# Performance work log

Measured on AMD Instinct MI355X. Metric: run time of the kernel, lower is better.

## Reference

```python
import jax, jax.numpy as jnp
import numpy as np

K = 7          # involution kernel size
G = 16         # groups = channels // group_channels = 256 // 16
BN_EPS = 1e-3  # Keras BatchNormalization default epsilon


def setup_inputs() -> dict:
    key = jax.random.key(0)
    ks = jax.random.split(key, 6)
    B, H, W, C = 4, 56, 56, 256
    Cr = C // 4                      # reduction_ratio = 4
    x = jax.random.normal(ks[0], (B, H, W, C), dtype=jnp.float32)
    w_reduce = jax.random.normal(ks[1], (C, Cr), dtype=jnp.float32) * (1.0 / np.sqrt(C))
    gamma = jnp.ones((Cr,), dtype=jnp.float32)
    beta = jnp.zeros((Cr,), dtype=jnp.float32)
    mean = jax.random.normal(ks[2], (Cr,), dtype=jnp.float32) * 0.1
    var = jax.random.uniform(ks[3], (Cr,), dtype=jnp.float32) + 0.5
    w_span = jax.random.normal(ks[4], (Cr, K * K * G), dtype=jnp.float32) * (1.0 / np.sqrt(Cr))
    b_span = jnp.zeros((K * K * G,), dtype=jnp.float32)
    return {"x": x, "w_reduce": w_reduce, "gamma": gamma, "beta": beta,
            "mean": mean, "var": var, "w_span": w_span, "b_span": b_span}


def reference(x, w_reduce, gamma, beta, mean, var, w_span, b_span):
    B, H, W, C = x.shape
    Cg = C // G  # channels per group
    # kernel generation branch: 1x1 conv -> BN (inference) -> ReLU -> 1x1 conv
    r = jnp.einsum('bhwc,cd->bhwd', x, w_reduce)
    r = jax.nn.relu((r - mean) * (gamma / jnp.sqrt(var + BN_EPS)) + beta)
    kgen = jnp.einsum('bhwd,de->bhwe', r, w_span) + b_span      # (B,H,W,K*K*G)
    kgen = kgen.reshape(B, H, W, G, K * K)
    # im2col with SAME padding (stride=1, pad (K-1)//2 symmetric), depth order (kh, kw, C)
    p = (K - 1) // 2
    xp = jnp.pad(x, ((0, 0), (p, p), (p, p), (0, 0)))
    patches = jnp.stack([xp[:, i:i + H, j:j + W, :]
                         for i in range(K) for j in range(K)], axis=3)  # (B,H,W,K*K,C)
    patches = patches.reshape(B, H, W, K * K, G, Cg)
    # per-pixel, per-group weighted reduction over the K*K window
    out = jnp.einsum('bhwgk,bhwkgc->bhwgc', kgen, patches)
    return out.reshape(B, H, W, C)
```

## Files before the change

### kernel.cpp

```cpp
#include <hip/hip_runtime.h>
#include <hip/hip_bf16.h>
#include <stdint.h>

#define B_   4
#define H_   56
#define W_   56
#define C_   256
#define CR   64
#define G_   16
#define CG   16
#define KS   7
#define KK   49
#define PADR 3
#define NPX  (B_*H_*W_)

typedef __attribute__((ext_vector_type(8))) short bf16x8;
typedef __attribute__((ext_vector_type(4))) float f32x4;
typedef __attribute__((ext_vector_type(2))) float f32x2;

__device__ __forceinline__ uint32_t f2bf(float f) {
    uint32_t x = __float_as_uint(f);
    return (x + 0x7fffu + ((x >> 16) & 1u)) >> 16;
}
__device__ __forceinline__ uint32_t pkbf(float a, float b) {
    union { __hip_bfloat162 h; uint32_t u; } c;
    c.h = __float22bfloat162_rn(make_float2(a, b));
    return c.u;
}
__device__ __forceinline__ float blo(uint32_t w) { return __uint_as_float(w << 16); }
__device__ __forceinline__ float bhi(uint32_t w) { return __uint_as_float(w & 0xffff0000u); }

union U4V { uint4 u; bf16x8 v; };

__global__ __launch_bounds__(256) void k0_prepack(
        const float* __restrict__ wr, const float* __restrict__ wspan,
        const float* __restrict__ gamma, const float* __restrict__ beta,
        const float* __restrict__ mean, const float* __restrict__ var,
        uint16_t* __restrict__ wrp, uint16_t* __restrict__ wpp,
        float* __restrict__ scale, float* __restrict__ shift) {
    int idx = blockIdx.x * 256 + threadIdx.x;
    {
        int j = idx & 7, lane = (idx >> 3) & 63, nb = (idx >> 9) & 3,
            kb = (idx >> 11) & 1, g = idx >> 12;
        int k = kb * 32 + (lane >> 4) * 8 + j;
        int n = nb * 16 + (lane & 15);
        float v = (n < KK) ? wspan[k * (KK * G_) + g * KK + n] : 0.f;
        wpp[idx] = (uint16_t)f2bf(v);
    }
    if (idx < 16384) {
        int j = idx & 7, lane = (idx >> 3) & 63, nb = (idx >> 9) & 3, kb = idx >> 11;
        int k = kb * 32 + (lane >> 4) * 8 + j;
        int n = nb * 16 + (lane & 15);
        wrp[idx] = (uint16_t)f2bf(wr[k * CR + n]);
    }
    if (idx < CR) {
        float s = gamma[idx] * rsqrtf(var[idx] + 1e-3f);
        scale[idx] = s;
        shift[idx] = beta[idx] - mean[idx] * s;
    }
}

__global__ __launch_bounds__(64) void k1_reduce(
        const float* __restrict__ x, const uint16_t* __restrict__ wrp,
        const float* __restrict__ scale, const float* __restrict__ shift,
        uint16_t* __restrict__ r) {
    int lane = threadIdx.x;
    int mt = blockIdx.x;
    int pix = mt * 16 + (lane & 15);
    const float* xrow = x + (size_t)pix * C_ + (lane >> 4) * 8;
    f32x4 acc[4] = {{0,0,0,0},{0,0,0,0},{0,0,0,0},{0,0,0,0}};
    for (int kb = 0; kb < 8; ++kb) {
        float4 a0 = *(const float4*)(xrow + kb * 32);
        float4 a1 = *(const float4*)(xrow + kb * 32 + 4);
        U4V af;
        af.u = make_uint4(pkbf(a0.x, a0.y), pkbf(a0.z, a0.w),
                          pkbf(a1.x, a1.y), pkbf(a1.z, a1.w));
        const uint16_t* wb = wrp + kb * 2048 + lane * 8;
        #pragma unroll
        for (int nb = 0; nb < 4; ++nb) {
            bf16x8 bf_ = *(const bf16x8*)(wb + nb * 512);
            acc[nb] = __builtin_amdgcn_mfma_f32_16x16x32_bf16(af.v, bf_, acc[nb], 0, 0, 0);
        }
    }
    int rq = (lane >> 4) * 4;
    #pragma unroll
    for (int nb = 0; nb < 4; ++nb) {
        int d = nb * 16 + (lane & 15);
        float s = scale[d], sh = shift[d];
        #pragma unroll
        for (int rg = 0; rg < 4; ++rg) {
            float v = fmaf(acc[nb][rg], s, sh);
            v = v > 0.f ? v : 0.f;
            r[(size_t)(mt * 16 + rq + rg) * CR + d] = (uint16_t)f2bf(v);
        }
    }
}

#define TS   14
#define HS   20
#define XSW  24
#define XROW (21*XSW)
#define KGW  56

__global__ __launch_bounds__(256, 3) void k2_involution(
        const float* __restrict__ x, const uint16_t* __restrict__ r,
        const uint16_t* __restrict__ wpp, const float* __restrict__ bspan,
        float* __restrict__ out) {
    __shared__ __align__(16) uint16_t xs[HS * XROW];
    __shared__ __align__(16) uint16_t kg[208 * KGW];

    int tid  = threadIdx.x;
    int tile = blockIdx.x, g = blockIdx.y, b = blockIdx.z;
    int ty0 = (tile >> 2) * TS, tx0 = (tile & 3) * TS;

    #pragma unroll
    for (int pass = 0; pass < 2; ++pass) {
        int i = tid + pass * 256;
        if (i < HS * HS) {
            int py = i / HS, px = i % HS;
            int gy = ty0 + py - PADR, gx = tx0 + px - PADR;
            uint4 wA = make_uint4(0, 0, 0, 0), wB = wA;
            if (gy >= 0 && gy < H_ && gx >= 0 && gx < W_) {
                const float* xp = x + (((size_t)(b * H_ + gy)) * W_ + gx) * C_ + g * CG;
                float4 v0 = *(const float4*)(xp + 0);
                float4 v1 = *(const float4*)(xp + 4);
                float4 v2 = *(const float4*)(xp + 8);
                float4 v3 = *(const float4*)(xp + 12);
                wA = make_uint4(pkbf(v0.x, v0.y), pkbf(v0.z, v0.w),
                                pkbf(v1.x, v1.y), pkbf(v1.z, v1.w));
                wB = make_uint4(pkbf(v2.x, v2.y), pkbf(v2.z, v2.w),
                                pkbf(v3.x, v3.y), pkbf(v3.z, v3.w));
            }
            uint16_t* dst = xs + py * XROW + px * XSW;
            *(uint4*)(dst + 0) = wA;
            *(uint4*)(dst + 8) = wB;
        }
    }

    int lane = tid & 63, w = tid >> 6;
    bf16x8 bfr[2][4];
    const uint16_t* wb = wpp + g * 4096 + lane * 8;
    #pragma unroll
    for (int kb = 0; kb < 2; ++kb)
        #pragma unroll
        for (int nb = 0; nb < 4; ++nb)
            bfr[kb][nb] = *(const bf16x8*)(wb + kb * 2048 + nb * 512);
    float bias[4];
    #pragma unroll
    for (int nb = 0; nb < 4; ++nb) {
        int n = nb * 16 + (lane & 15);
        bias[nb] = (n < KK) ? bspan[g * KK + n] : 0.f;
    }
    for (int mi = 0; mi < 4; ++mi) {
        int mt = mi * 4 + w;
        if (mt < 13) {
            int m  = mt * 16 + (lane & 15);
            int mm = m < 196 ? m : 195;
            int ly = mm / TS, lx = mm % TS;
            size_t pix = ((size_t)(b * H_ + ty0 + ly)) * W_ + (tx0 + lx);
            const uint16_t* rp = r + pix * CR + (lane >> 4) * 8;
            bf16x8 a0 = *(const bf16x8*)(rp);
            bf16x8 a1 = *(const bf16x8*)(rp + 32);
            f32x4 acc[4];
            #pragma unroll
            for (int nb = 0; nb < 4; ++nb)
                acc[nb] = (f32x4){bias[nb], bias[nb], bias[nb], bias[nb]};
            #pragma unroll
            for (int nb = 0; nb < 4; ++nb) {
                acc[nb] = __builtin_amdgcn_mfma_f32_16x16x32_bf16(a0, bfr[0][nb], acc[nb], 0, 0, 0);
                acc[nb] = __builtin_amdgcn_mfma_f32_16x16x32_bf16(a1, bfr[1][nb], acc[nb], 0, 0, 0);
            }
            #pragma unroll
            for (int nb = 0; nb < 4; ++nb) {
                int n = nb * 16 + (lane & 15);
                if (n < KK) {
                    int row = mt * 16 + (lane >> 4) * 4;
                    #pragma unroll
                    for (int rg = 0; rg < 4; ++rg)
                        kg[(row + rg) * KGW + n] = (uint16_t)f2bf(acc[nb][rg]);
                }
            }
        }
    }
    __syncthreads();

    if (tid < 196) {
        int p = tid >> 1, h = tid & 1;
        int ty = p / 7, tx = (p % 7) * 2;
        int rowL = ty * TS + tx;

        uint32_t kwL[28], kwR[28];
        #pragma unroll
        for (int t = 0; t < 7; ++t) {
            uint4 a = *(const uint4*)(kg + rowL * KGW + t * 8);
            uint4 c = *(const uint4*)(kg + (rowL + 1) * KGW + t * 8);
            kwL[t*4+0] = a.x; kwL[t*4+1] = a.y; kwL[t*4+2] = a.z; kwL[t*4+3] = a.w;
            kwR[t*4+0] = c.x; kwR[t*4+1] = c.y; kwR[t*4+2] = c.z; kwR[t*4+3] = c.w;
        }

        f32x2 accL[4] = {{0,0},{0,0},{0,0},{0,0}};
        f32x2 accR[4] = {{0,0},{0,0},{0,0},{0,0}};
        #pragma unroll
        for (int kh = 0; kh < KS; ++kh) {
            const uint16_t* xrow = xs + (ty + kh) * XROW + tx * XSW + h * 8;
            #pragma unroll
            for (int j = 0; j < 8; ++j) {
                uint4 xw = *(const uint4*)(xrow + j * XSW);
                float kvL = 0.f, kvR = 0.f;
                if (j < 7) { int t = kh * 7 + j;     kvL = (t & 1) ? bhi(kwL[t>>1]) : blo(kwL[t>>1]); }
                if (j > 0) { int t = kh * 7 + j - 1; kvR = (t & 1) ? bhi(kwR[t>>1]) : blo(kwR[t>>1]); }
                f32x2 kL = {kvL, kvL}, kR = {kvR, kvR};
                f32x2 x0 = {blo(xw.x), bhi(xw.x)};
                f32x2 x1 = {blo(xw.y), bhi(xw.y)};
                f32x2 x2 = {blo(xw.z), bhi(xw.z)};
                f32x2 x3 = {blo(xw.w), bhi(xw.w)};
                accL[0] = __builtin_elementwise_fma(kL, x0, accL[0]);
                accL[1] = __builtin_elementwise_fma(kL, x1, accL[1]);
                accL[2] = __builtin_elementwise_fma(kL, x2, accL[2]);
                accL[3] = __builtin_elementwise_fma(kL, x3, accL[3]);
                accR[0] = __builtin_elementwise_fma(kR, x0, accR[0]);
                accR[1] = __builtin_elementwise_fma(kR, x1, accR[1]);
                accR[2] = __builtin_elementwise_fma(kR, x2, accR[2]);
                accR[3] = __builtin_elementwise_fma(kR, x3, accR[3]);
            }
        }
        size_t pixL = ((size_t)(b * H_ + ty0 + ty)) * W_ + (tx0 + tx);
        float* opL = out + pixL * C_ + g * CG + h * 8;
        float* opR = opL + C_;
        *(float4*)(opL + 0) = make_float4(accL[0].x, accL[0].y, accL[1].x, accL[1].y);
        *(float4*)(opL + 4) = make_float4(accL[2].x, accL[2].y, accL[3].x, accL[3].y);
        *(float4*)(opR + 0) = make_float4(accR[0].x, accR[0].y, accR[1].x, accR[1].y);
        *(float4*)(opR + 4) = make_float4(accR[2].x, accR[2].y, accR[3].x, accR[3].y);
    }
}

extern "C" void kernel_launch(void* const* d_in, const int* in_sizes, int n_in,
                              void* d_out, int out_size, void* d_ws, size_t ws_size,
                              hipStream_t stream) {
    const float* x        = (const float*)d_in[0];
    const float* w_reduce = (const float*)d_in[1];
    const float* gamma    = (const float*)d_in[2];
    const float* beta     = (const float*)d_in[3];
    const float* mean     = (const float*)d_in[4];
    const float* var      = (const float*)d_in[5];
    const float* w_span   = (const float*)d_in[6];
    const float* b_span   = (const float*)d_in[7];
    float* out = (float*)d_out;

    uint8_t* ws = (uint8_t*)d_ws;
    uint16_t* r_ws  = (uint16_t*)(ws + 0);
    uint16_t* wrp   = (uint16_t*)(ws + 1605632);
    uint16_t* wpp   = (uint16_t*)(ws + 1638400);
    float*    scale = (float*)   (ws + 1769472);
    float*    shift = (float*)   (ws + 1769728);

    hipLaunchKernelGGL(k0_prepack, dim3(256), dim3(256), 0, stream,
                       w_reduce, w_span, gamma, beta, mean, var,
                       wrp, wpp, scale, shift);
    hipLaunchKernelGGL(k1_reduce, dim3(NPX / 16), dim3(64), 0, stream,
                       x, wrp, scale, shift, r_ws);
    hipLaunchKernelGGL(k2_involution, dim3(16, 16, B_), dim3(256), 0, stream,
                       x, r_ws, wpp, b_span, out);
}
```

Measured before the change: 100.1 us.

## Emit bf16 copy of x in reduce kernel and shrink involution LDS footprint

The reduce kernel now writes a bf16 copy of x while it is already converting it, and the involution kernel loads that copy instead of re-reading and converting fp32 x, which cuts its halo-load traffic in half. The reduce kernel packs four waves per block. The LDS layout is compacted (x stride 16, kgen 196 rows with per-row padding), occupancy is raised to 4 blocks per SIMD, and kernel weights are read per kh row from LDS instead of being held in 56 registers. The cost is an extra bf16 write of x to workspace, plus more LDS reads and possible bank conflicts from the unpadded x stride.

```diff
diff --git a/kernel.cpp b/kernel.cpp
--- a/kernel.cpp
+++ b/kernel.cpp
@@ -60,14 +60,16 @@
     }
 }
 
-__global__ __launch_bounds__(64) void k1_reduce(
+__global__ __launch_bounds__(256) void k1_reduce(
         const float* __restrict__ x, const uint16_t* __restrict__ wrp,
         const float* __restrict__ scale, const float* __restrict__ shift,
-        uint16_t* __restrict__ r) {
-    int lane = threadIdx.x;
-    int mt = blockIdx.x;
+        uint16_t* __restrict__ r, uint16_t* __restrict__ xbf) {
+    int tid = threadIdx.x;
+    int lane = tid & 63, w = tid >> 6;
+    int mt = blockIdx.x * 4 + w;
     int pix = mt * 16 + (lane & 15);
-    const float* xrow = x + (size_t)pix * C_ + (lane >> 4) * 8;
+    int ko = (lane >> 4) * 8;
+    const float* xrow = x + (size_t)pix * C_ + ko;
     f32x4 acc[4] = {{0,0,0,0},{0,0,0,0},{0,0,0,0},{0,0,0,0}};
     for (int kb = 0; kb < 8; ++kb) {
         float4 a0 = *(const float4*)(xrow + kb * 32);
@@ -75,6 +77,7 @@
         U4V af;
         af.u = make_uint4(pkbf(a0.x, a0.y), pkbf(a0.z, a0.w),
                           pkbf(a1.x, a1.y), pkbf(a1.z, a1.w));
+        *(uint4*)(xbf + (size_t)pix * C_ + ko + kb * 32) = af.u;
         const uint16_t* wb = wrp + kb * 2048 + lane * 8;
         #pragma unroll
         for (int nb = 0; nb < 4; ++nb) {
@@ -98,16 +101,15 @@
 
 #define TS   14
 #define HS   20
-#define XSW  24
-#define XROW (21*XSW)
+#define XSW  16
 #define KGW  56
 
-__global__ __launch_bounds__(256, 3) void k2_involution(
-        const float* __restrict__ x, const uint16_t* __restrict__ r,
+__global__ __launch_bounds__(256, 4) void k2_involution(
+        const uint16_t* __restrict__ xbf, const uint16_t* __restrict__ r,
         const uint16_t* __restrict__ wpp, const float* __restrict__ bspan,
         float* __restrict__ out) {
-    __shared__ __align__(16) uint16_t xs[HS * XROW];
-    __shared__ __align__(16) uint16_t kg[208 * KGW];
+    __shared__ __align__(16) uint16_t xs[HS * HS * XSW];
+    __shared__ __align__(16) uint16_t kg[196 * KGW];
 
     int tid  = threadIdx.x;
     int tile = blockIdx.x, g = blockIdx.y, b = blockIdx.z;
@@ -121,17 +123,11 @@
             int gy = ty0 + py - PADR, gx = tx0 + px - PADR;
             uint4 wA = make_uint4(0, 0, 0, 0), wB = wA;
             if (gy >= 0 && gy < H_ && gx >= 0 && gx < W_) {
-                const float* xp = x + (((size_t)(b * H_ + gy)) * W_ + gx) * C_ + g * CG;
-                float4 v0 = *(const float4*)(xp + 0);
-                float4 v1 = *(const float4*)(xp + 4);
-                float4 v2 = *(const float4*)(xp + 8);
-                float4 v3 = *(const float4*)(xp + 12);
-                wA = make_uint4(pkbf(v0.x, v0.y), pkbf(v0.z, v0.w),
-                                pkbf(v1.x, v1.y), pkbf(v1.z, v1.w));
-                wB = make_uint4(pkbf(v2.x, v2.y), pkbf(v2.z, v2.w),
-                                pkbf(v3.x, v3.y), pkbf(v3.z, v3.w));
-            }
-            uint16_t* dst = xs + py * XROW + px * XSW;
+                const uint16_t* xp = xbf + (((size_t)(b * H_ + gy)) * W_ + gx) * C_ + g * CG;
+                wA = *(const uint4*)(xp);
+                wB = *(const uint4*)(xp + 8);
+            }
+            uint16_t* dst = xs + i * XSW;
             *(uint4*)(dst + 0) = wA;
             *(uint4*)(dst + 8) = wB;
         }
@@ -170,14 +166,17 @@
                 acc[nb] = __builtin_amdgcn_mfma_f32_16x16x32_bf16(a0, bfr[0][nb], acc[nb], 0, 0, 0);
                 acc[nb] = __builtin_amdgcn_mfma_f32_16x16x32_bf16(a1, bfr[1][nb], acc[nb], 0, 0, 0);
             }
-            #pragma unroll
-            for (int nb = 0; nb < 4; ++nb) {
-                int n = nb * 16 + (lane & 15);
-                if (n < KK) {
-                    int row = mt * 16 + (lane >> 4) * 4;
-                    #pragma unroll
-                    for (int rg = 0; rg < 4; ++rg)
-                        kg[(row + rg) * KGW + n] = (uint16_t)f2bf(acc[nb][rg]);
+            int row = mt * 16 + (lane >> 4) * 4;
+            if (row < 196) {
+                #pragma unroll
+                for (int nb = 0; nb < 4; ++nb) {
+                    int n = nb * 16 + (lane & 15);
+                    if (n < KK) {
+                        int slot = n + n / 7;
+                        #pragma unroll
+                        for (int rg = 0; rg < 4; ++rg)
+                            kg[(row + rg) * KGW + slot] = (uint16_t)f2bf(acc[nb][rg]);
+                    }
                 }
             }
         }
@@ -187,28 +186,24 @@
     if (tid < 196) {
         int p = tid >> 1, h = tid & 1;
         int ty = p / 7, tx = (p % 7) * 2;
-        int rowL = ty * TS + tx;
-
-        uint32_t kwL[28], kwR[28];
-        #pragma unroll
-        for (int t = 0; t < 7; ++t) {
-            uint4 a = *(const uint4*)(kg + rowL * KGW + t * 8);
-            uint4 c = *(const uint4*)(kg + (rowL + 1) * KGW + t * 8);
-            kwL[t*4+0] = a.x; kwL[t*4+1] = a.y; kwL[t*4+2] = a.z; kwL[t*4+3] = a.w;
-            kwR[t*4+0] = c.x; kwR[t*4+1] = c.y; kwR[t*4+2] = c.z; kwR[t*4+3] = c.w;
-        }
+        const uint16_t* kgL = kg + (ty * TS + tx) * KGW;
+        const uint16_t* kgR = kgL + KGW;
 
         f32x2 accL[4] = {{0,0},{0,0},{0,0},{0,0}};
         f32x2 accR[4] = {{0,0},{0,0},{0,0},{0,0}};
         #pragma unroll
         for (int kh = 0; kh < KS; ++kh) {
-            const uint16_t* xrow = xs + (ty + kh) * XROW + tx * XSW + h * 8;
+            uint4 aL = *(const uint4*)(kgL + kh * 8);
+            uint4 aR = *(const uint4*)(kgR + kh * 8);
+            const uint32_t kwL[4] = {aL.x, aL.y, aL.z, aL.w};
+            const uint32_t kwR[4] = {aR.x, aR.y, aR.z, aR.w};
+            const uint16_t* xrow = xs + ((ty + kh) * HS + tx) * XSW + h * 8;
             #pragma unroll
             for (int j = 0; j < 8; ++j) {
                 uint4 xw = *(const uint4*)(xrow + j * XSW);
                 float kvL = 0.f, kvR = 0.f;
-                if (j < 7) { int t = kh * 7 + j;     kvL = (t & 1) ? bhi(kwL[t>>1]) : blo(kwL[t>>1]); }
-                if (j > 0) { int t = kh * 7 + j - 1; kvR = (t & 1) ? bhi(kwR[t>>1]) : blo(kwR[t>>1]); }
+                if (j < 7) kvL = (j & 1) ? bhi(kwL[j >> 1]) : blo(kwL[j >> 1]);
+                if (j > 0) { int t = j - 1; kvR = (t & 1) ? bhi(kwR[t >> 1]) : blo(kwR[t >> 1]); }
                 f32x2 kL = {kvL, kvL}, kR = {kvR, kvR};
                 f32x2 x0 = {blo(xw.x), bhi(xw.x)};
                 f32x2 x1 = {blo(xw.y), bhi(xw.y)};
@@ -253,12 +248,13 @@
     uint16_t* wpp   = (uint16_t*)(ws + 1638400);
     float*    scale = (float*)   (ws + 1769472);
     float*    shift = (float*)   (ws + 1769728);
+    uint16_t* xbf   = (uint16_t*)(ws + 1769984);
 
     hipLaunchKernelGGL(k0_prepack, dim3(256), dim3(256), 0, stream,
                        w_reduce, w_span, gamma, beta, mean, var,
                        wrp, wpp, scale, shift);
-    hipLaunchKernelGGL(k1_reduce, dim3(NPX / 16), dim3(64), 0, stream,
-                       x, wrp, scale, shift, r_ws);
+    hipLaunchKernelGGL(k1_reduce, dim3(NPX / 64), dim3(256), 0, stream,
+                       x, wrp, scale, shift, r_ws, xbf);
     hipLaunchKernelGGL(k2_involution, dim3(16, 16, B_), dim3(256), 0, stream,
-                       x, r_ws, wpp, b_span, out);
-}
+                       xbf, r_ws, wpp, b_span, out);
+}
```

Measured after the change: 99.07 us. About the same (-1.0%).
